# Kernel optimization log

Hardware: AMD Instinct MI355X
Metric: run time of the kernel (lower is better)

## Reference

```python
import jax, jax.numpy as jnp
import numpy as np

N_NODES = 100000
N_EDGES = 1600000
F_IN = 128
OUT = 32
PERIODS = 12


def setup_inputs() -> dict:
    key = jax.random.key(0)
    ks = jax.random.split(key, 12)
    s = 0.05
    return {
        'x': jax.random.normal(ks[0], (N_NODES, F_IN, PERIODS), jnp.float32),
        'edge_index': jax.random.randint(ks[1], (2, N_EDGES), 0, N_NODES, dtype=jnp.int64),
        'Wz': jax.random.normal(ks[2], (F_IN, OUT), jnp.float32) * s,
        'bz': jnp.zeros((OUT,), jnp.float32),
        'Lz': jax.random.normal(ks[3], (2 * OUT, OUT), jnp.float32) * s,
        'lbz': jnp.zeros((OUT,), jnp.float32),
        'Wh': jax.random.normal(ks[4], (F_IN, OUT), jnp.float32) * s,
        'bh': jnp.zeros((OUT,), jnp.float32),
        'Lh': jax.random.normal(ks[5], (2 * OUT, OUT), jnp.float32) * s,
        'lbh': jnp.zeros((OUT,), jnp.float32),
        'att': jax.random.normal(ks[6], (PERIODS,), jnp.float32),
        'Wlin': jax.random.normal(ks[7], (OUT, PERIODS), jnp.float32) * s,
        'blin': jnp.zeros((PERIODS,), jnp.float32),
    }


def _gcn_norm(edge_index, n):
    # GCNConv normalization with self loops: D^-1/2 (A+I) D^-1/2
    loop = jnp.arange(n, dtype=edge_index.dtype)
    row = jnp.concatenate([edge_index[0], loop])  # sources
    col = jnp.concatenate([edge_index[1], loop])  # targets
    deg = jax.ops.segment_sum(jnp.ones(row.shape[0], jnp.float32), col, num_segments=n)
    dis = jnp.where(deg > 0, jax.lax.rsqrt(deg), 0.0)
    return row, col, dis[row] * dis[col]


def reference(x, edge_index, Wz, bz, Lz, lbz, Wh, bh, Lh, lbh, att, Wlin, blin):
    n = x.shape[0]
    row, col, norm = _gcn_norm(edge_index, n)
    probs = jax.nn.softmax(att)
    xP = jnp.transpose(x, (2, 0, 1))  # [P, N, F]
    H0 = jnp.zeros((n, OUT), x.dtype)

    def conv(xp, W, b):
        xw = xp @ W                              # [N, OUT]
        msg = xw[row] * norm[:, None]            # gather at source
        return jax.ops.segment_sum(msg, col, num_segments=n) + b

    def step(acc, inp):
        xp, p = inp
        # TGCN cell with H=0 (A3TGCN passes H=None each period)
        Z = jax.nn.sigmoid(jnp.concatenate([conv(xp, Wz, bz), H0], axis=1) @ Lz + lbz)
        Ht = jnp.tanh(jnp.concatenate([conv(xp, Wh, bh), H0], axis=1) @ Lh + lbh)
        Hp = (1.0 - Z) * Ht                      # Z*H + (1-Z)*Ht with H=0
        return acc + p * Hp, None

    acc, _ = jax.lax.scan(step, H0, (xP, probs))
    h = jax.nn.relu(acc)
    return h @ Wlin + blin
```

## Files before the change

kernel.cpp:

```cpp
#include <hip/hip_runtime.h>
#include <hip/hip_fp16.h>

#define N_NODES 100000
#define N_EDGES 1600000
#define F_IN 128
#define OUT 32
#define PERIODS 12

__global__ void k_prep(const float* __restrict__ Wz, const float* __restrict__ bz,
                       const float* __restrict__ Lz, const float* __restrict__ lbz,
                       const float* __restrict__ Wh, const float* __restrict__ bh,
                       const float* __restrict__ Lh, const float* __restrict__ lbh,
                       const float* __restrict__ att,
                       float* __restrict__ M, float* __restrict__ cc,
                       float* __restrict__ probs) {
    int t = threadIdx.x;
    for (int idx = t; idx < F_IN * 64; idx += 256) {
        int f = idx >> 6, c = idx & 63;
        const float* W = (c < 32) ? Wz : Wh;
        const float* L = (c < 32) ? Lz : Lh;
        int cj = c & 31;
        float s = 0.f;
        #pragma unroll 8
        for (int j = 0; j < 32; ++j) s += W[f * 32 + j] * L[j * 32 + cj];
        M[idx] = s;
    }
    if (t < 64) {
        int c = t & 31;
        const float* b  = (t < 32) ? bz : bh;
        const float* L  = (t < 32) ? Lz : Lh;
        const float* lb = (t < 32) ? lbz : lbh;
        float s = lb[c];
        for (int j = 0; j < 32; ++j) s += b[j] * L[j * 32 + c];
        cc[t] = s;
    }
    if (t == 0) {
        float m = att[0];
        for (int p = 1; p < PERIODS; ++p) m = fmaxf(m, att[p]);
        float e[PERIODS]; float sum = 0.f;
        for (int p = 0; p < PERIODS; ++p) { e[p] = expf(att[p] - m); sum += e[p]; }
        for (int p = 0; p < PERIODS; ++p) probs[p] = e[p] / sum;
    }
}

__global__ void k_count(const int* __restrict__ ei, int* __restrict__ cnt) {
    int e = blockIdx.x * 256 + threadIdx.x;
    if (e < N_EDGES) {
        int c = ei[N_EDGES + e];
        if ((unsigned)c < N_NODES) atomicAdd(&cnt[c], 1);
    }
}

__global__ void k_dis(const int* __restrict__ cnt, float* __restrict__ dis) {
    int i = blockIdx.x * 256 + threadIdx.x;
    if (i < N_NODES) dis[i] = rsqrtf((float)(cnt[i] + 1));
}

__global__ void k_scan1(const int* __restrict__ cnt, int* __restrict__ rp,
                        int* __restrict__ partials) {
    __shared__ int s[256];
    int t = threadIdx.x;
    int i = blockIdx.x * 256 + t;
    int v = (i < N_NODES) ? cnt[i] : 0;
    s[t] = v;
    __syncthreads();
    for (int off = 1; off < 256; off <<= 1) {
        int y = (t >= off) ? s[t - off] : 0;
        __syncthreads();
        s[t] += y;
        __syncthreads();
    }
    if (i < N_NODES) rp[i] = s[t] - v;
    if (t == 255) partials[blockIdx.x] = s[255];
}

__global__ void k_scan2(int* __restrict__ partials, int np) {
    __shared__ int s[512];
    int t = threadIdx.x;
    int v = (t < np) ? partials[t] : 0;
    s[t] = v;
    __syncthreads();
    for (int off = 1; off < 512; off <<= 1) {
        int y = (t >= off) ? s[t - off] : 0;
        __syncthreads();
        s[t] += y;
        __syncthreads();
    }
    if (t < np) partials[t] = s[t] - v;
}

__global__ void k_scan3(int* __restrict__ rp, const int* __restrict__ partials) {
    int i = blockIdx.x * 256 + threadIdx.x;
    if (i < N_NODES) rp[i] += partials[blockIdx.x];
    if (i == 0) rp[N_NODES] = N_EDGES;
}

__global__ void k_fill(const int* __restrict__ ei, const int* __restrict__ rp,
                       int* __restrict__ cnt, int* __restrict__ srcIdx) {
    int e = blockIdx.x * 256 + threadIdx.x;
    if (e < N_EDGES) {
        int c = ei[N_EDGES + e];
        int r = ei[e];
        if ((unsigned)c < N_NODES) {
            int pos = rp[c] + atomicSub(&cnt[c], 1) - 1;
            srcIdx[pos] = r;
        }
    }
}

__global__ __launch_bounds__(256, 3) void k_proj4(const float* __restrict__ x,
                                                  const float* __restrict__ M,
                                                  __half* __restrict__ U) {
    __shared__ float sM[F_IN * 64];
    int t = threadIdx.x;

    {
        const float4* Mv = reinterpret_cast<const float4*>(M);
        float4* sMv = reinterpret_cast<float4*>(sM);
        #pragma unroll
        for (int i = 0; i < 8; ++i) sMv[t + 256 * i] = Mv[t + 256 * i];
    }
    __syncthreads();

    int lane = t & 63;
    int wv = t >> 6;
    int node = blockIdx.x * 32 + wv * 8 + (lane >> 3);
    int co = lane & 7;

    const float4* xg4 = reinterpret_cast<const float4*>(x + (size_t)node * (F_IN * PERIODS));

    float acc[8][PERIODS];
    #pragma unroll
    for (int c = 0; c < 8; ++c)
        #pragma unroll
        for (int p = 0; p < PERIODS; ++p) acc[c][p] = 0.f;

    for (int f = 0; f < F_IN; ++f) {
        float4 xa = xg4[f * 3 + 0];
        float4 xb = xg4[f * 3 + 1];
        float4 xc = xg4[f * 3 + 2];
        float4 m0 = *reinterpret_cast<const float4*>(&sM[f * 64 + co * 8]);
        float4 m1 = *reinterpret_cast<const float4*>(&sM[f * 64 + co * 8 + 4]);
        float xv[PERIODS] = {xa.x, xa.y, xa.z, xa.w,
                             xb.x, xb.y, xb.z, xb.w,
                             xc.x, xc.y, xc.z, xc.w};
        float mm[8] = {m0.x, m0.y, m0.z, m0.w, m1.x, m1.y, m1.z, m1.w};
        #pragma unroll
        for (int c = 0; c < 8; ++c)
            #pragma unroll
            for (int p = 0; p < PERIODS; ++p)
                acc[c][p] = fmaf(mm[c], xv[p], acc[c][p]);
    }

    __half* un = U + (size_t)node * 768 + co * 8;
    #pragma unroll
    for (int p = 0; p < PERIODS; ++p) {
        union { uint4 u; __half2 h[4]; } r;
        r.h[0] = __floats2half2_rn(acc[0][p], acc[1][p]);
        r.h[1] = __floats2half2_rn(acc[2][p], acc[3][p]);
        r.h[2] = __floats2half2_rn(acc[4][p], acc[5][p]);
        r.h[3] = __floats2half2_rn(acc[6][p], acc[7][p]);
        *reinterpret_cast<uint4*>(un + p * 64) = r.u;
    }
}

__global__ void k_agg(const __half* __restrict__ U, const int* __restrict__ rp,
                      const int* __restrict__ srcIdx, const float* __restrict__ dis,
                      const float* __restrict__ cc, const float* __restrict__ probs,
                      const float* __restrict__ Wlin, const float* __restrict__ blin,
                      float* __restrict__ out) {
    int n = blockIdx.x;
    int t = threadIdx.x;
    float dn = dis[n];

    float a0, a1, a2, a3;
    {
        union { uint2 u; __half2 h[2]; } r;
        r.u = reinterpret_cast<const uint2*>(U + (size_t)n * 768)[t];
        float2 f0 = __half22float2(r.h[0]);
        float2 f1 = __half22float2(r.h[1]);
        float w = dn * dn;
        a0 = w * f0.x; a1 = w * f0.y; a2 = w * f1.x; a3 = w * f1.y;
    }
    int beg = rp[n], end = rp[n + 1];
    int e = beg;
    for (; e + 3 < end; e += 4) {
        int s0 = srcIdx[e], s1 = srcIdx[e + 1], s2 = srcIdx[e + 2], s3 = srcIdx[e + 3];
        float w0 = dis[s0] * dn, w1 = dis[s1] * dn, w2 = dis[s2] * dn, w3 = dis[s3] * dn;
        union { uint2 u; __half2 h[2]; } r0, r1, r2, r3;
        r0.u = reinterpret_cast<const uint2*>(U + (size_t)s0 * 768)[t];
        r1.u = reinterpret_cast<const uint2*>(U + (size_t)s1 * 768)[t];
        r2.u = reinterpret_cast<const uint2*>(U + (size_t)s2 * 768)[t];
        r3.u = reinterpret_cast<const uint2*>(U + (size_t)s3 * 768)[t];
        float2 f0, f1;
        f0 = __half22float2(r0.h[0]); f1 = __half22float2(r0.h[1]);
        a0 += w0 * f0.x; a1 += w0 * f0.y; a2 += w0 * f1.x; a3 += w0 * f1.y;
        f0 = __half22float2(r1.h[0]); f1 = __half22float2(r1.h[1]);
        a0 += w1 * f0.x; a1 += w1 * f0.y; a2 += w1 * f1.x; a3 += w1 * f1.y;
        f0 = __half22float2(r2.h[0]); f1 = __half22float2(r2.h[1]);
        a0 += w2 * f0.x; a1 += w2 * f0.y; a2 += w2 * f1.x; a3 += w2 * f1.y;
        f0 = __half22float2(r3.h[0]); f1 = __half22float2(r3.h[1]);
        a0 += w3 * f0.x; a1 += w3 * f0.y; a2 += w3 * f1.x; a3 += w3 * f1.y;
    }
    for (; e < end; ++e) {
        int s = srcIdx[e];
        float w = dis[s] * dn;
        union { uint2 u; __half2 h[2]; } r;
        r.u = reinterpret_cast<const uint2*>(U + (size_t)s * 768)[t];
        float2 f0 = __half22float2(r.h[0]);
        float2 f1 = __half22float2(r.h[1]);
        a0 += w * f0.x; a1 += w * f0.y; a2 += w * f1.x; a3 += w * f1.y;
    }

    __shared__ float sacc[768];
    __shared__ float sterm[PERIODS * 32];
    __shared__ float shf[32];
    sacc[4 * t + 0] = a0; sacc[4 * t + 1] = a1;
    sacc[4 * t + 2] = a2; sacc[4 * t + 3] = a3;
    __syncthreads();

    for (int w2 = t; w2 < PERIODS * 32; w2 += 192) {
        int p = w2 >> 5, c = w2 & 31;
        float z = sacc[p * 64 + c]      + cc[c];
        float h = sacc[p * 64 + 32 + c] + cc[32 + c];
        float zs = 1.f / (1.f + __expf(-z));
        sterm[w2] = probs[p] * (1.f - zs) * tanhf(h);
    }
    __syncthreads();

    if (t < 32) {
        float s = 0.f;
        #pragma unroll
        for (int p = 0; p < PERIODS; ++p) s += sterm[p * 32 + t];
        shf[t] = fmaxf(s, 0.f);
    }
    __syncthreads();

    if (t < PERIODS) {
        float o = blin[t];
        #pragma unroll 8
        for (int c = 0; c < OUT; ++c) o += shf[c] * Wlin[c * PERIODS + t];
        out[(size_t)n * PERIODS + t] = o;
    }
}

extern "C" void kernel_launch(void* const* d_in, const int* in_sizes, int n_in,
                              void* d_out, int out_size, void* d_ws, size_t ws_size,
                              hipStream_t stream) {
    const float* x    = (const float*)d_in[0];
    const int*   ei   = (const int*)d_in[1];
    const float* Wz   = (const float*)d_in[2];
    const float* bz   = (const float*)d_in[3];
    const float* Lz   = (const float*)d_in[4];
    const float* lbz  = (const float*)d_in[5];
    const float* Wh   = (const float*)d_in[6];
    const float* bh   = (const float*)d_in[7];
    const float* Lh   = (const float*)d_in[8];
    const float* lbh  = (const float*)d_in[9];
    const float* att  = (const float*)d_in[10];
    const float* Wlin = (const float*)d_in[11];
    const float* blin = (const float*)d_in[12];
    float* out = (float*)d_out;

    char* w = (char*)d_ws;
    size_t off = 0;
    __half* U      = (__half*)(w + off); off += (size_t)N_NODES * 768 * 2;
    float*  M      = (float*)(w + off);  off += 128 * 64 * 4;
    float*  cc     = (float*)(w + off);  off += 256;
    float*  probs  = (float*)(w + off);  off += 64;
    float*  dis    = (float*)(w + off);  off += N_NODES * 4;
    int*    cnt    = (int*)(w + off);    off += N_NODES * 4;
    int*    rp     = (int*)(w + off);    off += (N_NODES + 1) * 4 + 12;
    int*    parts  = (int*)(w + off);    off += 2048;
    int*    srcIdx = (int*)(w + off);    off += (size_t)N_EDGES * 4;
    (void)ws_size; (void)in_sizes; (void)n_in; (void)out_size;

    const int SCAN_BLOCKS = (N_NODES + 255) / 256;

    hipMemsetAsync(cnt, 0, N_NODES * 4, stream);

    k_prep<<<1, 256, 0, stream>>>(Wz, bz, Lz, lbz, Wh, bh, Lh, lbh, att, M, cc, probs);
    k_count<<<(N_EDGES + 255) / 256, 256, 0, stream>>>(ei, cnt);
    k_dis<<<SCAN_BLOCKS, 256, 0, stream>>>(cnt, dis);
    k_scan1<<<SCAN_BLOCKS, 256, 0, stream>>>(cnt, rp, parts);
    k_scan2<<<1, 512, 0, stream>>>(parts, SCAN_BLOCKS);
    k_scan3<<<SCAN_BLOCKS, 256, 0, stream>>>(rp, parts);
    k_fill<<<(N_EDGES + 255) / 256, 256, 0, stream>>>(ei, rp, cnt, srcIdx);
    k_proj4<<<N_NODES / 32, 256, 0, stream>>>(x, M, U);
    k_agg<<<N_NODES, 192, 0, stream>>>(U, rp, srcIdx, dis, cc, probs, Wlin, blin, out);
}
```

Before: 836.9 us.

## Aggregate one node per wavefront and stream x with nontemporal loads

The aggregation kernel now maps one node to a single 64-lane wavefront, packing four nodes per 256-thread block, instead of one 192-thread block per node. Each lane accumulates twelve values across three chunks, and the gate/readout epilogue is reorganised per wave. The projection kernel reads x with nontemporal loads and unrolls its feature loop by two to reduce cache pollution from the large streaming input. The gather now issues smaller half2 loads per lane, which may change coalescing efficiency.

Result: slower. 980.1 us (+17.1%).

```diff
diff --git a/kernel.cpp b/kernel.cpp
--- a/kernel.cpp
+++ b/kernel.cpp
@@ -6,6 +6,8 @@
 #define F_IN 128
 #define OUT 32
 #define PERIODS 12
+
+typedef float f32x4 __attribute__((ext_vector_type(4)));
 
 __global__ void k_prep(const float* __restrict__ Wz, const float* __restrict__ bz,
                        const float* __restrict__ Lz, const float* __restrict__ lbz,
@@ -127,7 +129,7 @@
     int node = blockIdx.x * 32 + wv * 8 + (lane >> 3);
     int co = lane & 7;
 
-    const float4* xg4 = reinterpret_cast<const float4*>(x + (size_t)node * (F_IN * PERIODS));
+    const f32x4* xg4 = reinterpret_cast<const f32x4*>(x + (size_t)node * (F_IN * PERIODS));
 
     float acc[8][PERIODS];
     #pragma unroll
@@ -135,10 +137,11 @@
         #pragma unroll
         for (int p = 0; p < PERIODS; ++p) acc[c][p] = 0.f;
 
+    #pragma unroll 2
     for (int f = 0; f < F_IN; ++f) {
-        float4 xa = xg4[f * 3 + 0];
-        float4 xb = xg4[f * 3 + 1];
-        float4 xc = xg4[f * 3 + 2];
+        f32x4 xa = __builtin_nontemporal_load(&xg4[f * 3 + 0]);
+        f32x4 xb = __builtin_nontemporal_load(&xg4[f * 3 + 1]);
+        f32x4 xc = __builtin_nontemporal_load(&xg4[f * 3 + 2]);
         float4 m0 = *reinterpret_cast<const float4*>(&sM[f * 64 + co * 8]);
         float4 m1 = *reinterpret_cast<const float4*>(&sM[f * 64 + co * 8 + 4]);
         float xv[PERIODS] = {xa.x, xa.y, xa.z, xa.w,
@@ -164,83 +167,115 @@
     }
 }
 
-__global__ void k_agg(const __half* __restrict__ U, const int* __restrict__ rp,
-                      const int* __restrict__ srcIdx, const float* __restrict__ dis,
-                      const float* __restrict__ cc, const float* __restrict__ probs,
-                      const float* __restrict__ Wlin, const float* __restrict__ blin,
-                      float* __restrict__ out) {
-    int n = blockIdx.x;
-    int t = threadIdx.x;
+__global__ __launch_bounds__(256, 4) void k_agg2(
+        const __half* __restrict__ U, const int* __restrict__ rp,
+        const int* __restrict__ srcIdx, const float* __restrict__ dis,
+        const float* __restrict__ cc, const float* __restrict__ probs,
+        const float* __restrict__ Wlin, const float* __restrict__ blin,
+        float* __restrict__ out) {
+    int t = threadIdx.x;
+    int wv = t >> 6;
+    int L  = t & 63;
+    int n = blockIdx.x * 4 + wv;
+
     float dn = dis[n];
-
-    float a0, a1, a2, a3;
+    float acc[12];
+
     {
-        union { uint2 u; __half2 h[2]; } r;
-        r.u = reinterpret_cast<const uint2*>(U + (size_t)n * 768)[t];
-        float2 f0 = __half22float2(r.h[0]);
-        float2 f1 = __half22float2(r.h[1]);
+        const __half2* row = reinterpret_cast<const __half2*>(U + (size_t)n * 768);
         float w = dn * dn;
-        a0 = w * f0.x; a1 = w * f0.y; a2 = w * f1.x; a3 = w * f1.y;
-    }
+        #pragma unroll
+        for (int j = 0; j < 3; ++j) {
+            __half2 h0 = row[j * 128 + 2 * L];
+            __half2 h1 = row[j * 128 + 2 * L + 1];
+            float2 f0 = __half22float2(h0);
+            float2 f1 = __half22float2(h1);
+            acc[j * 4 + 0] = w * f0.x; acc[j * 4 + 1] = w * f0.y;
+            acc[j * 4 + 2] = w * f1.x; acc[j * 4 + 3] = w * f1.y;
+        }
+    }
+
     int beg = rp[n], end = rp[n + 1];
     int e = beg;
     for (; e + 3 < end; e += 4) {
         int s0 = srcIdx[e], s1 = srcIdx[e + 1], s2 = srcIdx[e + 2], s3 = srcIdx[e + 3];
         float w0 = dis[s0] * dn, w1 = dis[s1] * dn, w2 = dis[s2] * dn, w3 = dis[s3] * dn;
-        union { uint2 u; __half2 h[2]; } r0, r1, r2, r3;
-        r0.u = reinterpret_cast<const uint2*>(U + (size_t)s0 * 768)[t];
-        r1.u = reinterpret_cast<const uint2*>(U + (size_t)s1 * 768)[t];
-        r2.u = reinterpret_cast<const uint2*>(U + (size_t)s2 * 768)[t];
-        r3.u = reinterpret_cast<const uint2*>(U + (size_t)s3 * 768)[t];
-        float2 f0, f1;
-        f0 = __half22float2(r0.h[0]); f1 = __half22float2(r0.h[1]);
-        a0 += w0 * f0.x; a1 += w0 * f0.y; a2 += w0 * f1.x; a3 += w0 * f1.y;
-        f0 = __half22float2(r1.h[0]); f1 = __half22float2(r1.h[1]);
-        a0 += w1 * f0.x; a1 += w1 * f0.y; a2 += w1 * f1.x; a3 += w1 * f1.y;
-        f0 = __half22float2(r2.h[0]); f1 = __half22float2(r2.h[1]);
-        a0 += w2 * f0.x; a1 += w2 * f0.y; a2 += w2 * f1.x; a3 += w2 * f1.y;
-        f0 = __half22float2(r3.h[0]); f1 = __half22float2(r3.h[1]);
-        a0 += w3 * f0.x; a1 += w3 * f0.y; a2 += w3 * f1.x; a3 += w3 * f1.y;
+        const __half2* r0 = reinterpret_cast<const __half2*>(U + (size_t)s0 * 768);
+        const __half2* r1 = reinterpret_cast<const __half2*>(U + (size_t)s1 * 768);
+        const __half2* r2 = reinterpret_cast<const __half2*>(U + (size_t)s2 * 768);
+        const __half2* r3 = reinterpret_cast<const __half2*>(U + (size_t)s3 * 768);
+        #pragma unroll
+        for (int j = 0; j < 3; ++j) {
+            __half2 a0 = r0[j * 128 + 2 * L], b0 = r0[j * 128 + 2 * L + 1];
+            __half2 a1 = r1[j * 128 + 2 * L], b1 = r1[j * 128 + 2 * L + 1];
+            __half2 a2 = r2[j * 128 + 2 * L], b2 = r2[j * 128 + 2 * L + 1];
+            __half2 a3 = r3[j * 128 + 2 * L], b3 = r3[j * 128 + 2 * L + 1];
+            float2 f0, f1;
+            f0 = __half22float2(a0); f1 = __half22float2(b0);
+            acc[j*4+0] += w0 * f0.x; acc[j*4+1] += w0 * f0.y;
+            acc[j*4+2] += w0 * f1.x; acc[j*4+3] += w0 * f1.y;
+            f0 = __half22float2(a1); f1 = __half22float2(b1);
+            acc[j*4+0] += w1 * f0.x; acc[j*4+1] += w1 * f0.y;
+            acc[j*4+2] += w1 * f1.x; acc[j*4+3] += w1 * f1.y;
+            f0 = __half22float2(a2); f1 = __half22float2(b2);
+            acc[j*4+0] += w2 * f0.x; acc[j*4+1] += w2 * f0.y;
+            acc[j*4+2] += w2 * f1.x; acc[j*4+3] += w2 * f1.y;
+            f0 = __half22float2(a3); f1 = __half22float2(b3);
+            acc[j*4+0] += w3 * f0.x; acc[j*4+1] += w3 * f0.y;
+            acc[j*4+2] += w3 * f1.x; acc[j*4+3] += w3 * f1.y;
+        }
     }
     for (; e < end; ++e) {
         int s = srcIdx[e];
         float w = dis[s] * dn;
-        union { uint2 u; __half2 h[2]; } r;
-        r.u = reinterpret_cast<const uint2*>(U + (size_t)s * 768)[t];
-        float2 f0 = __half22float2(r.h[0]);
-        float2 f1 = __half22float2(r.h[1]);
-        a0 += w * f0.x; a1 += w * f0.y; a2 += w * f1.x; a3 += w * f1.y;
-    }
-
-    __shared__ float sacc[768];
-    __shared__ float sterm[PERIODS * 32];
-    __shared__ float shf[32];
-    sacc[4 * t + 0] = a0; sacc[4 * t + 1] = a1;
-    sacc[4 * t + 2] = a2; sacc[4 * t + 3] = a3;
-    __syncthreads();
-
-    for (int w2 = t; w2 < PERIODS * 32; w2 += 192) {
-        int p = w2 >> 5, c = w2 & 31;
-        float z = sacc[p * 64 + c]      + cc[c];
-        float h = sacc[p * 64 + 32 + c] + cc[32 + c];
+        const __half2* r = reinterpret_cast<const __half2*>(U + (size_t)s * 768);
+        #pragma unroll
+        for (int j = 0; j < 3; ++j) {
+            __half2 h0 = r[j * 128 + 2 * L];
+            __half2 h1 = r[j * 128 + 2 * L + 1];
+            float2 f0 = __half22float2(h0);
+            float2 f1 = __half22float2(h1);
+            acc[j*4+0] += w * f0.x; acc[j*4+1] += w * f0.y;
+            acc[j*4+2] += w * f1.x; acc[j*4+3] += w * f1.y;
+        }
+    }
+
+    __shared__ float sacc[4][768];
+    __shared__ float sterm[4][PERIODS * 32];
+    __shared__ float shf[4][32];
+    #pragma unroll
+    for (int j = 0; j < 3; ++j) {
+        sacc[wv][j * 256 + 4 * L + 0] = acc[j * 4 + 0];
+        sacc[wv][j * 256 + 4 * L + 1] = acc[j * 4 + 1];
+        sacc[wv][j * 256 + 4 * L + 2] = acc[j * 4 + 2];
+        sacc[wv][j * 256 + 4 * L + 3] = acc[j * 4 + 3];
+    }
+    __syncthreads();
+
+    #pragma unroll
+    for (int i = 0; i < 6; ++i) {
+        int idx = L * 6 + i;
+        int p = idx >> 5, c = idx & 31;
+        float z = sacc[wv][p * 64 + c]      + cc[c];
+        float h = sacc[wv][p * 64 + 32 + c] + cc[32 + c];
         float zs = 1.f / (1.f + __expf(-z));
-        sterm[w2] = probs[p] * (1.f - zs) * tanhf(h);
-    }
-    __syncthreads();
-
-    if (t < 32) {
+        sterm[wv][idx] = probs[p] * (1.f - zs) * tanhf(h);
+    }
+    __syncthreads();
+
+    if (L < 32) {
         float s = 0.f;
         #pragma unroll
-        for (int p = 0; p < PERIODS; ++p) s += sterm[p * 32 + t];
-        shf[t] = fmaxf(s, 0.f);
-    }
-    __syncthreads();
-
-    if (t < PERIODS) {
-        float o = blin[t];
+        for (int p = 0; p < PERIODS; ++p) s += sterm[wv][p * 32 + L];
+        shf[wv][L] = fmaxf(s, 0.f);
+    }
+    __syncthreads();
+
+    if (L < PERIODS) {
+        float o = blin[L];
         #pragma unroll 8
-        for (int c = 0; c < OUT; ++c) o += shf[c] * Wlin[c * PERIODS + t];
-        out[(size_t)n * PERIODS + t] = o;
+        for (int c = 0; c < OUT; ++c) o += shf[wv][c] * Wlin[c * PERIODS + L];
+        out[(size_t)n * PERIODS + L] = o;
     }
 }
 
@@ -277,7 +312,7 @@
 
     const int SCAN_BLOCKS = (N_NODES + 255) / 256;
 
-    hipMemsetAsync(cnt, 0, N_NODES * 4, stream);
+    (void)hipMemsetAsync(cnt, 0, N_NODES * 4, stream);
 
     k_prep<<<1, 256, 0, stream>>>(Wz, bz, Lz, lbz, Wh, bh, Lh, lbh, att, M, cc, probs);
     k_count<<<(N_EDGES + 255) / 256, 256, 0, stream>>>(ei, cnt);
@@ -287,5 +322,5 @@
     k_scan3<<<SCAN_BLOCKS, 256, 0, stream>>>(rp, parts);
     k_fill<<<(N_EDGES + 255) / 256, 256, 0, stream>>>(ei, rp, cnt, srcIdx);
     k_proj4<<<N_NODES / 32, 256, 0, stream>>>(x, M, U);
-    k_agg<<<N_NODES, 192, 0, stream>>>(U, rp, srcIdx, dis, cc, probs, Wlin, blin, out);
-}
+    k_agg2<<<N_NODES / 4, 256, 0, stream>>>(U, rp, srcIdx, dis, cc, probs, Wlin, blin, out);
+}
```

## Stage x tiles in shared memory and read projection weights wave-uniformly

Applied to the files above, without the earlier changes.

The projection kernel now loads 64-node chunks of x into padded LDS in coalesced float4 loads, 16 features at a time, instead of each thread streaming its own node's row directly from global memory. Each wave owns one output-column group, so the weight values are wave-uniform and read from global memory, which can become scalar loads. The goal is better coalescing of the dominant 51 MB x read and less LDS traffic for weights. The cost is eight barrier-separated staging phases per block and larger blocks with high register use.

Measured after the change: 1.769 ms. 111% more time.

```diff
diff --git a/kernel.cpp b/kernel.cpp
--- a/kernel.cpp
+++ b/kernel.cpp
@@ -108,26 +108,18 @@
     }
 }
 
-__global__ __launch_bounds__(256, 3) void k_proj4(const float* __restrict__ x,
+#define XSTR 196
+__global__ __launch_bounds__(512, 4) void k_proj5(const float* __restrict__ x,
                                                   const float* __restrict__ M,
                                                   __half* __restrict__ U) {
-    __shared__ float sM[F_IN * 64];
-    int t = threadIdx.x;
-
-    {
-        const float4* Mv = reinterpret_cast<const float4*>(M);
-        float4* sMv = reinterpret_cast<float4*>(sM);
-        #pragma unroll
-        for (int i = 0; i < 8; ++i) sMv[t + 256 * i] = Mv[t + 256 * i];
-    }
-    __syncthreads();
-
-    int lane = t & 63;
-    int wv = t >> 6;
-    int node = blockIdx.x * 32 + wv * 8 + (lane >> 3);
-    int co = lane & 7;
-
-    const float4* xg4 = reinterpret_cast<const float4*>(x + (size_t)node * (F_IN * PERIODS));
+    __shared__ float sx[64 * XSTR];
+    int t = threadIdx.x;
+    int L = t & 63;
+    int co = __builtin_amdgcn_readfirstlane(t >> 6);
+    int nb0 = blockIdx.x * 64;
+    int node = nb0 + L;
+
+    const float4* xg = reinterpret_cast<const float4*>(x);
 
     float acc[8][PERIODS];
     #pragma unroll
@@ -135,32 +127,50 @@
         #pragma unroll
         for (int p = 0; p < PERIODS; ++p) acc[c][p] = 0.f;
 
-    for (int f = 0; f < F_IN; ++f) {
-        float4 xa = xg4[f * 3 + 0];
-        float4 xb = xg4[f * 3 + 1];
-        float4 xc = xg4[f * 3 + 2];
-        float4 m0 = *reinterpret_cast<const float4*>(&sM[f * 64 + co * 8]);
-        float4 m1 = *reinterpret_cast<const float4*>(&sM[f * 64 + co * 8 + 4]);
-        float xv[PERIODS] = {xa.x, xa.y, xa.z, xa.w,
-                             xb.x, xb.y, xb.z, xb.w,
-                             xc.x, xc.y, xc.z, xc.w};
-        float mm[8] = {m0.x, m0.y, m0.z, m0.w, m1.x, m1.y, m1.z, m1.w};
+    for (int kc = 0; kc < 8; ++kc) {
+        __syncthreads();
         #pragma unroll
-        for (int c = 0; c < 8; ++c)
+        for (int i = 0; i < 6; ++i) {
+            int j = t + 512 * i;
+            int g = j / 48;
+            int wi = j - g * 48;
+            int gsrc = nb0 + g; if (gsrc >= N_NODES) gsrc = N_NODES - 1;
+            *reinterpret_cast<float4*>(&sx[g * XSTR + wi * 4]) =
+                xg[(size_t)gsrc * 384 + kc * 48 + wi];
+        }
+        __syncthreads();
+
+        #pragma unroll 4
+        for (int fi = 0; fi < 16; ++fi) {
+            int f = kc * 16 + fi;
+            float4 m0 = *reinterpret_cast<const float4*>(&M[f * 64 + co * 8]);
+            float4 m1 = *reinterpret_cast<const float4*>(&M[f * 64 + co * 8 + 4]);
+            float4 x0 = *reinterpret_cast<const float4*>(&sx[L * XSTR + fi * 12 + 0]);
+            float4 x1 = *reinterpret_cast<const float4*>(&sx[L * XSTR + fi * 12 + 4]);
+            float4 x2 = *reinterpret_cast<const float4*>(&sx[L * XSTR + fi * 12 + 8]);
+            float mm[8] = {m0.x, m0.y, m0.z, m0.w, m1.x, m1.y, m1.z, m1.w};
+            float xv[PERIODS] = {x0.x, x0.y, x0.z, x0.w,
+                                 x1.x, x1.y, x1.z, x1.w,
+                                 x2.x, x2.y, x2.z, x2.w};
             #pragma unroll
-            for (int p = 0; p < PERIODS; ++p)
-                acc[c][p] = fmaf(mm[c], xv[p], acc[c][p]);
-    }
-
-    __half* un = U + (size_t)node * 768 + co * 8;
-    #pragma unroll
-    for (int p = 0; p < PERIODS; ++p) {
-        union { uint4 u; __half2 h[4]; } r;
-        r.h[0] = __floats2half2_rn(acc[0][p], acc[1][p]);
-        r.h[1] = __floats2half2_rn(acc[2][p], acc[3][p]);
-        r.h[2] = __floats2half2_rn(acc[4][p], acc[5][p]);
-        r.h[3] = __floats2half2_rn(acc[6][p], acc[7][p]);
-        *reinterpret_cast<uint4*>(un + p * 64) = r.u;
+            for (int c = 0; c < 8; ++c)
+                #pragma unroll
+                for (int p = 0; p < PERIODS; ++p)
+                    acc[c][p] = fmaf(mm[c], xv[p], acc[c][p]);
+        }
+    }
+
+    if (node < N_NODES) {
+        __half* un = U + (size_t)node * 768 + co * 8;
+        #pragma unroll
+        for (int p = 0; p < PERIODS; ++p) {
+            union { uint4 u; __half2 h[4]; } r;
+            r.h[0] = __floats2half2_rn(acc[0][p], acc[1][p]);
+            r.h[1] = __floats2half2_rn(acc[2][p], acc[3][p]);
+            r.h[2] = __floats2half2_rn(acc[4][p], acc[5][p]);
+            r.h[3] = __floats2half2_rn(acc[6][p], acc[7][p]);
+            *reinterpret_cast<uint4*>(un + p * 64) = r.u;
+        }
     }
 }
 
@@ -277,7 +287,7 @@
 
     const int SCAN_BLOCKS = (N_NODES + 255) / 256;
 
-    hipMemsetAsync(cnt, 0, N_NODES * 4, stream);
+    (void)hipMemsetAsync(cnt, 0, N_NODES * 4, stream);
 
     k_prep<<<1, 256, 0, stream>>>(Wz, bz, Lz, lbz, Wh, bh, Lh, lbh, att, M, cc, probs);
     k_count<<<(N_EDGES + 255) / 256, 256, 0, stream>>>(ei, cnt);
@@ -286,6 +296,6 @@
     k_scan2<<<1, 512, 0, stream>>>(parts, SCAN_BLOCKS);
     k_scan3<<<SCAN_BLOCKS, 256, 0, stream>>>(rp, parts);
     k_fill<<<(N_EDGES + 255) / 256, 256, 0, stream>>>(ei, rp, cnt, srcIdx);
-    k_proj4<<<N_NODES / 32, 256, 0, stream>>>(x, M, U);
+    k_proj5<<<(N_NODES + 63) / 64, 512, 0, stream>>>(x, M, U);
     k_agg<<<N_NODES, 192, 0, stream>>>(U, rp, srcIdx, dis, cc, probs, Wlin, blin, out);
 }
```
